# Kernel optimization log

Hardware: AMD Instinct MI355X
Metric: run time of the kernel (lower is better)

The kernel has to match this reference:

```python
import jax, jax.numpy as jnp
import numpy as np

N = 50000      # users
F_IN = 768     # input features
H = 128        # hidden_dimension == linear_channels
E = 400000     # edges per relation
SQRT_D = float(np.sqrt(H))  # heads=1 -> d = H


def leaky_relu(x):
    return jnp.where(x >= 0, x, 0.01 * x)


def hgt_layer(x, edge_list, Wk, bk, Wq, bq, Wv, bv, rel_params, Wa, ba, skip):
    # x: [N, H]; edge_list: list of [2, E] int arrays (row0=src, row1=dst)
    n = x.shape[0]
    k = x @ Wk + bk
    q = x @ Wq + bq
    v = x @ Wv + bv
    out = jnp.zeros_like(x)
    for ei, (A, M, p) in zip(edge_list, rel_params):
        src, dst = ei[0], ei[1]
        kr = (k @ A)[src]                                  # [E, H] gather
        vr = (v @ M)[src]                                  # [E, H] gather
        alpha = jnp.sum(q[dst] * kr, axis=-1) * p[0] / SQRT_D  # [E]
        amax = jax.ops.segment_max(alpha, dst, num_segments=n)
        ex = jnp.exp(alpha - amax[dst])
        denom = jax.ops.segment_sum(ex, dst, num_segments=n)
        w = ex / denom[dst]                                # segment softmax per dst
        out = out + jax.ops.segment_sum(vr * w[:, None], dst, num_segments=n)
    out = jax.nn.gelu(out, approximate=False) @ Wa + ba
    beta = jax.nn.sigmoid(skip[0])                          # learnable skip gate
    return beta * out + (1.0 - beta) * x


def setup_inputs() -> dict:
    key = jax.random.key(0)
    ks = jax.random.split(key, 16)
    d = {}
    d['features'] = jax.random.normal(ks[0], (N, F_IN), dtype=jnp.float32)
    d['edge_index0'] = jax.random.randint(ks[1], (2, E), 0, N, dtype=jnp.int64)
    d['edge_index1'] = jax.random.randint(ks[2], (2, E), 0, N, dtype=jnp.int64)
    d['W1'] = jax.random.normal(ks[3], (F_IN, H), dtype=jnp.float32) / np.sqrt(F_IN)
    d['b1'] = jnp.zeros((H,), jnp.float32)
    d['Wk'] = jax.random.normal(ks[4], (H, H), dtype=jnp.float32) / np.sqrt(H)
    d['bk'] = jnp.zeros((H,), jnp.float32)
    d['Wq'] = jax.random.normal(ks[5], (H, H), dtype=jnp.float32) / np.sqrt(H)
    d['bq'] = jnp.zeros((H,), jnp.float32)
    d['Wv'] = jax.random.normal(ks[6], (H, H), dtype=jnp.float32) / np.sqrt(H)
    d['bv'] = jnp.zeros((H,), jnp.float32)
    d['A0'] = jax.random.normal(ks[7], (H, H), dtype=jnp.float32) / np.sqrt(H)
    d['M0'] = jax.random.normal(ks[8], (H, H), dtype=jnp.float32) / np.sqrt(H)
    d['p0'] = jnp.ones((1,), jnp.float32)
    d['A1'] = jax.random.normal(ks[9], (H, H), dtype=jnp.float32) / np.sqrt(H)
    d['M1'] = jax.random.normal(ks[10], (H, H), dtype=jnp.float32) / np.sqrt(H)
    d['p1'] = jnp.ones((1,), jnp.float32)
    d['Wa'] = jax.random.normal(ks[11], (H, H), dtype=jnp.float32) / np.sqrt(H)
    d['ba'] = jnp.zeros((H,), jnp.float32)
    d['skip'] = jnp.ones((1,), jnp.float32)
    d['Wo1'] = jax.random.normal(ks[12], (H, 64), dtype=jnp.float32) / np.sqrt(H)
    d['bo1'] = jnp.zeros((64,), jnp.float32)
    d['Wo2'] = jax.random.normal(ks[13], (64, 2), dtype=jnp.float32) / np.sqrt(64)
    d['bo2'] = jnp.zeros((2,), jnp.float32)
    return d


def reference(features, edge_index0, edge_index1, W1, b1, Wk, bk, Wq, bq, Wv, bv,
              A0, M0, p0, A1, M1, p1, Wa, ba, skip, Wo1, bo1, Wo2, bo2):
    edges = [edge_index0, edge_index1]
    rel_params = [(A0, M0, p0), (A1, M1, p1)]
    # linear1 + LeakyReLU (dropout is identity in eval mode)
    x = leaky_relu(features @ W1 + b1)
    # HGT_layer1 applied twice (as in the original forward)
    x = hgt_layer(x, edges, Wk, bk, Wq, bq, Wv, bv, rel_params, Wa, ba, skip)
    x = hgt_layer(x, edges, Wk, bk, Wq, bq, Wv, bv, rel_params, Wa, ba, skip)
    x = leaky_relu(x @ Wo1 + bo1)
    return x @ Wo2 + bo2
```

## Files before the change

### kernel.cpp

```cpp
#include <hip/hip_runtime.h>
#include <math.h>

#define NNODES 50000
#define FIN 768
#define HDIM 128
#define NEDGE 400000
#define NSB 49

typedef _Float16 half8 __attribute__((ext_vector_type(8)));
typedef _Float16 half4 __attribute__((ext_vector_type(4)));
typedef _Float16 half2v __attribute__((ext_vector_type(2)));
typedef float f32x4 __attribute__((ext_vector_type(4)));

__device__ __forceinline__ void gld_lds16(const void* g, void* l) {
    __builtin_amdgcn_global_load_lds((const __attribute__((address_space(1))) unsigned int*)g,
                                     (__attribute__((address_space(3))) unsigned int*)l, 16, 0, 0);
}


__global__ __launch_bounds__(256) void count2_kernel(const int* __restrict__ ei0, const int* __restrict__ ei1,
                                                     int* __restrict__ deg0, int* __restrict__ deg1) {
    int e = blockIdx.x * 256 + threadIdx.x;
    const int* ei = blockIdx.y ? ei1 : ei0;
    int* deg = blockIdx.y ? deg1 : deg0;
    if (e < NEDGE) atomicAdd(&deg[ei[NEDGE + e]], 1);
}

__global__ __launch_bounds__(1024) void scan1_kernel(const int* __restrict__ deg0, const int* __restrict__ deg1,
                                                     int* __restrict__ ptr0, int* __restrict__ ptr1,
                                                     int* __restrict__ sums) {
    const int r = blockIdx.y;
    const int* deg = r ? deg1 : deg0;
    int* ptr = r ? ptr1 : ptr0;
    const int b = blockIdx.x, t = threadIdx.x, i = b * 1024 + t;
    __shared__ int buf[1024];
    int v = (i < NNODES) ? deg[i] : 0;
    buf[t] = v;
    __syncthreads();
    for (int off = 1; off < 1024; off <<= 1) {
        int x = (t >= off) ? buf[t - off] : 0;
        __syncthreads();
        buf[t] += x;
        __syncthreads();
    }
    if (i < NNODES) ptr[i] = buf[t] - v;
    if (t == 1023) sums[r * 64 + b] = buf[1023];
}

__global__ __launch_bounds__(64) void scan2_kernel(int* __restrict__ sums,
                                                   int* __restrict__ ptr0, int* __restrict__ ptr1) {
    const int r = blockIdx.x, t = threadIdx.x;
    int orig = (t < NSB) ? sums[r * 64 + t] : 0;
    int v = orig;
    #pragma unroll
    for (int off = 1; off < 64; off <<= 1) {
        int u = __shfl_up(v, off, 64);
        if (t >= off) v += u;
    }
    if (t < NSB) sums[r * 64 + t] = v - orig;
    if (t == NSB - 1) (r ? ptr1 : ptr0)[NNODES] = v;
}

__global__ __launch_bounds__(1024) void scan3_kernel(const int* __restrict__ sums,
                                                     int* __restrict__ ptr0, int* __restrict__ ptr1) {
    const int r = blockIdx.y;
    int* ptr = r ? ptr1 : ptr0;
    const int i = blockIdx.x * 1024 + threadIdx.x;
    if (i < NNODES) ptr[i] += sums[r * 64 + blockIdx.x];
}

__global__ __launch_bounds__(256) void scatter2_kernel(const int* __restrict__ ei0, const int* __restrict__ ei1,
                                                       const int* __restrict__ ptr0, const int* __restrict__ ptr1,
                                                       int* __restrict__ fill0, int* __restrict__ fill1,
                                                       int* __restrict__ csr0, int* __restrict__ csr1) {
    int e = blockIdx.x * 256 + threadIdx.x;
    const int* ei = blockIdx.y ? ei1 : ei0;
    const int* ptr = blockIdx.y ? ptr1 : ptr0;
    int* fill = blockIdx.y ? fill1 : fill0;
    int* csr = blockIdx.y ? csr1 : csr0;
    if (e < NEDGE) {
        int s = ei[e], d = ei[NEDGE + e];
        int p = atomicAdd(&fill[d], 1);
        csr[ptr[d] + p] = s;
    }
}

__global__ __launch_bounds__(256) void gemm_cmb_kernel(
    const float* __restrict__ Wk, const float* __restrict__ Wv,
    const float* __restrict__ A0v, const float* __restrict__ M0v,
    const float* __restrict__ A1v, const float* __restrict__ M1v,
    float* __restrict__ WkA0, float* __restrict__ WvM0,
    float* __restrict__ WkA1, float* __restrict__ WvM1)
{
    const int z = blockIdx.z;
    const float* A = (z & 1) ? Wv : Wk;
    const float* B = (z == 0) ? A0v : (z == 1) ? M0v : (z == 2) ? A1v : M1v;
    float* C = (z == 0) ? WkA0 : (z == 1) ? WvM0 : (z == 2) ? WkA1 : WvM1;
    const int M = 128, N = 128, K = 128;
    __shared__ float As[16][64];
    __shared__ float Bs[16][64];
    const int t = threadIdx.x;
    const int tx = t & 15, ty = t >> 4;
    const int bm = blockIdx.x * 64, bn = blockIdx.y * 64;
    const int ar = t >> 2, ac = (t & 3) << 2;
    const int br = t >> 4, bc = (t & 15) << 2;
    float acc[4][4] = {};
    for (int kb = 0; kb < K; kb += 16) {
        float4 av = *reinterpret_cast<const float4*>(A + (size_t)(bm + ar) * K + kb + ac);
        float4 bv = *reinterpret_cast<const float4*>(B + (size_t)(kb + br) * N + bn + bc);
        __syncthreads();
        As[ac + 0][ar] = av.x; As[ac + 1][ar] = av.y; As[ac + 2][ar] = av.z; As[ac + 3][ar] = av.w;
        *reinterpret_cast<float4*>(&Bs[br][bc]) = bv;
        __syncthreads();
        #pragma unroll
        for (int kk = 0; kk < 16; ++kk) {
            float4 a = *reinterpret_cast<const float4*>(&As[kk][ty << 2]);
            float4 b = *reinterpret_cast<const float4*>(&Bs[kk][tx << 2]);
            float am[4] = {a.x, a.y, a.z, a.w};
            float bb[4] = {b.x, b.y, b.z, b.w};
            #pragma unroll
            for (int i = 0; i < 4; ++i)
                #pragma unroll
                for (int j = 0; j < 4; ++j)
                    acc[i][j] = fmaf(am[i], bb[j], acc[i][j]);
        }
    }
    #pragma unroll
    for (int i = 0; i < 4; ++i)
        #pragma unroll
        for (int j = 0; j < 4; ++j)
            C[(size_t)(bm + (ty << 2) + i) * N + bn + (tx << 2) + j] = acc[i][j];
}

__global__ __launch_bounds__(128) void bias_cmb_kernel(
    const float* __restrict__ bk, const float* __restrict__ bv,
    const float* __restrict__ A0v, const float* __restrict__ M0v,
    const float* __restrict__ A1v, const float* __restrict__ M1v,
    float* __restrict__ bqkv)
{
    const int z = blockIdx.x;
    const int j = threadIdx.x;
    const float* b = (z & 1) ? bv : bk;
    const float* Mtx = (z == 0) ? A0v : (z == 1) ? M0v : (z == 2) ? A1v : M1v;
    float s = 0.f;
    for (int i = 0; i < HDIM; ++i) s += b[i] * Mtx[i * HDIM + j];
    const int r = z >> 1, kv = z & 1;
    bqkv[128 + r * 256 + ((j >> 1) << 2) + (kv << 1) + (j & 1)] = s;
}

__global__ __launch_bounds__(128) void pack_qkvT(
    const float* __restrict__ Wq,   const float* __restrict__ WkA0, const float* __restrict__ WvM0,
    const float* __restrict__ WkA1, const float* __restrict__ WvM1,
    const float* __restrict__ bq,
    _Float16* __restrict__ WT, float* __restrict__ bb)
{
    int n = blockIdx.x;
    int k = threadIdx.x;
    int seg = n >> 7, col = n & 127;
    const float* W = (seg == 0) ? Wq : (seg == 1) ? WkA0 : (seg == 2) ? WvM0 : (seg == 3) ? WkA1 : WvM1;
    int np;
    if (seg == 0) np = col;
    else {
        int r = (seg - 1) >> 1, kv = (seg - 1) & 1;
        np = 128 + r * 256 + ((col >> 1) << 2) + (kv << 1) + (col & 1);
    }
    WT[(size_t)np * 128 + k] = (_Float16)W[(size_t)k * 128 + col];
    if (seg == 0 && k == 0) bb[col] = bq[col];
}

__global__ void transpose_h(const float* __restrict__ W, _Float16* __restrict__ WT, int K, int N) {
    int n = blockIdx.x, k = threadIdx.x;
    WT[(size_t)n * K + k] = (_Float16)W[(size_t)k * N + n];
}

template<int MODE, bool A_F32, bool GELU>
__global__ __launch_bounds__(256) void gemm_h(
    const void* __restrict__ Av, const _Float16* __restrict__ Bt,
    const float* __restrict__ bias, const _Float16* __restrict__ Dh,
    const float* __restrict__ gate, _Float16* __restrict__ C,
    int M, int N, int K)
{
    __shared__ _Float16 sA[4096];
    __shared__ _Float16 sB[4096];
    const int t = threadIdx.x;
    const int w = t >> 6, lane = t & 63;
    const int wm = w >> 1, wn = w & 1;
    const int bm = blockIdx.x * 128, bn = blockIdx.y * 128;
    const f32x4 zero = {0.f, 0.f, 0.f, 0.f};
    f32x4 acc[4][4];
    #pragma unroll
    for (int i = 0; i < 4; ++i)
        #pragma unroll
        for (int j = 0; j < 4; ++j) acc[i][j] = zero;

    for (int kb = 0; kb < K; kb += 32) {
        #pragma unroll
        for (int it = 0; it < 2; ++it) {
            const int c = it * 256 + t;
            const int l = c & 63;
            const int row = ((c >> 6) << 4) | (l & 15);
            const int kc = (l >> 4) << 3;
            const int cb = it * 256 + (t & 192);
            int arow = bm + row; if (arow > M - 1) arow = M - 1;
            int brow = bn + row; if (brow > N - 1) brow = N - 1;
            if (A_F32) {
                const float* ap = (const float*)Av + (size_t)arow * K + kb + kc;
                f32x4 v0 = *(const f32x4*)ap;
                f32x4 v1 = *(const f32x4*)(ap + 4);
                float tmp[8] = {v0[0], v0[1], v0[2], v0[3], v1[0], v1[1], v1[2], v1[3]};
                half8 av;
                #pragma unroll
                for (int j = 0; j < 8; ++j) {
                    float x = tmp[j];
                    if (GELU) x = 0.5f * x * (1.0f + erff(x * 0.70710678118654752f));
                    av[j] = (_Float16)x;
                }
                *(half8*)(sA + (size_t)c * 8) = av;
            } else {
                gld_lds16((const _Float16*)Av + (size_t)arow * K + kb + kc, sA + (size_t)cb * 8);
            }
            gld_lds16(Bt + (size_t)brow * K + kb + kc, sB + (size_t)cb * 8);
        }
        __syncthreads();
        half8 af[4], bf[4];
        #pragma unroll
        for (int i = 0; i < 4; ++i) af[i] = *(const half8*)(sA + ((size_t)((wm * 4 + i) * 64 + lane)) * 8);
        #pragma unroll
        for (int i = 0; i < 4; ++i) bf[i] = *(const half8*)(sB + ((size_t)((wn * 4 + i) * 64 + lane)) * 8);
        #pragma unroll
        for (int i = 0; i < 4; ++i)
            #pragma unroll
            for (int j = 0; j < 4; ++j)
                acc[i][j] = __builtin_amdgcn_mfma_f32_16x16x32_f16(af[i], bf[j], acc[i][j], 0, 0, 0);
        __syncthreads();
    }

    float be = 0.f;
    if (MODE == 2) be = 1.0f / (1.0f + __expf(-gate[0]));
    const int crow0 = bm + wm * 64;
    const int ccol0 = bn + wn * 64;
    #pragma unroll
    for (int i = 0; i < 4; ++i) {
        #pragma unroll
        for (int j = 0; j < 4; ++j) {
            const int col = ccol0 + j * 16 + (lane & 15);
            if (col >= N) continue;
            #pragma unroll
            for (int r = 0; r < 4; ++r) {
                const int row = crow0 + i * 16 + ((lane >> 4) << 2) + r;
                if (row >= M) continue;
                float val = acc[i][j][r] + bias[col];
                if (MODE == 1) val = (val >= 0.f) ? val : 0.01f * val;
                if (MODE == 2) val = be * val + (1.f - be) * (float)Dh[(size_t)row * HDIM + col];
                C[(size_t)row * N + col] = (_Float16)val;
            }
        }
    }
}

__global__ __launch_bounds__(256) void attn2_kernel(
    const _Float16* __restrict__ qkv,
    const int* __restrict__ ptr0, const int* __restrict__ csr0,
    const int* __restrict__ ptr1, const int* __restrict__ csr1,
    const float* __restrict__ p0, const float* __restrict__ p1,
    float* __restrict__ att)
{
    const int w = (blockIdx.x * 256 + threadIdx.x) >> 6;
    if (w >= NNODES) return;
    const int lane = threadIdx.x & 63;
    half2v qh = *(const half2v*)(qkv + (size_t)w * 640 + (lane << 1));
    const float qx = (float)qh[0], qy = (float)qh[1];
    float ox = 0.f, oy = 0.f;
    #pragma unroll
    for (int r = 0; r < 2; ++r) {
        const int* ptrv = r ? ptr1 : ptr0;
        const int* csr  = r ? csr1 : csr0;
        const float scale = (r ? p1[0] : p0[0]) * 0.08838834764831845f;
        const int start = ptrv[w], end = ptrv[w + 1];
        if (start == end) continue;
        const _Float16* tbl = qkv + 128 + 256 * r + (lane << 2);
        float denom = 0.f, ax = 0.f, ay = 0.f;
        int i = start;
        for (; i + 4 <= end; i += 4) {
            const int s0 = csr[i], s1 = csr[i + 1], s2 = csr[i + 2], s3 = csr[i + 3];
            half4 kv0 = *(const half4*)(tbl + (size_t)s0 * 640);
            half4 kv1 = *(const half4*)(tbl + (size_t)s1 * 640);
            half4 kv2 = *(const half4*)(tbl + (size_t)s2 * 640);
            half4 kv3 = *(const half4*)(tbl + (size_t)s3 * 640);
            float d0 = qx * (float)kv0[0] + qy * (float)kv0[1];
            float d1 = qx * (float)kv1[0] + qy * (float)kv1[1];
            float d2 = qx * (float)kv2[0] + qy * (float)kv2[1];
            float d3 = qx * (float)kv3[0] + qy * (float)kv3[1];
            #pragma unroll
            for (int o2 = 32; o2; o2 >>= 1) {
                d0 += __shfl_xor(d0, o2, 64);
                d1 += __shfl_xor(d1, o2, 64);
                d2 += __shfl_xor(d2, o2, 64);
                d3 += __shfl_xor(d3, o2, 64);
            }
            const float e0 = __expf(d0 * scale), e1 = __expf(d1 * scale);
            const float e2 = __expf(d2 * scale), e3 = __expf(d3 * scale);
            denom += (e0 + e1) + (e2 + e3);
            ax += e0 * (float)kv0[2] + e1 * (float)kv1[2] + e2 * (float)kv2[2] + e3 * (float)kv3[2];
            ay += e0 * (float)kv0[3] + e1 * (float)kv1[3] + e2 * (float)kv2[3] + e3 * (float)kv3[3];
        }
        for (; i < end; ++i) {
            const int s = csr[i];
            half4 kv = *(const half4*)(tbl + (size_t)s * 640);
            float d = qx * (float)kv[0] + qy * (float)kv[1];
            #pragma unroll
            for (int o2 = 32; o2; o2 >>= 1) d += __shfl_xor(d, o2, 64);
            const float e = __expf(d * scale);
            denom += e;
            ax += e * (float)kv[2];
            ay += e * (float)kv[3];
        }
        const float inv = 1.0f / denom;
        ox += ax * inv; oy += ay * inv;
    }
    *reinterpret_cast<float2*>(att + (size_t)w * HDIM + (lane << 1)) = make_float2(ox, oy);
}

__global__ __launch_bounds__(256) void head2_kernel(const _Float16* __restrict__ h,
                                                    const float* __restrict__ Wo2,
                                                    const float* __restrict__ bo2,
                                                    float* __restrict__ out)
{
    int i = blockIdx.x * 256 + threadIdx.x;
    if (i >= NNODES) return;
    const _Float16* hp = h + (size_t)i * 64;
    float s0 = bo2[0], s1 = bo2[1];
    #pragma unroll
    for (int j0 = 0; j0 < 64; j0 += 8) {
        half8 hv = *(const half8*)(hp + j0);
        #pragma unroll
        for (int j = 0; j < 8; ++j) {
            float v = (float)hv[j];
            s0 += v * Wo2[2 * (j0 + j)];
            s1 += v * Wo2[2 * (j0 + j) + 1];
        }
    }
    out[2 * i] = s0;
    out[2 * i + 1] = s1;
}


extern "C" void kernel_launch(void* const* d_in, const int* in_sizes, int n_in,
                              void* d_out, int out_size, void* d_ws, size_t ws_size,
                              hipStream_t stream)
{
    const float* features = (const float*)d_in[0];
    const int* ei0 = (const int*)d_in[1];
    const int* ei1 = (const int*)d_in[2];
    const float* W1 = (const float*)d_in[3];
    const float* b1 = (const float*)d_in[4];
    const float* Wk = (const float*)d_in[5];
    const float* bk = (const float*)d_in[6];
    const float* Wq = (const float*)d_in[7];
    const float* bq = (const float*)d_in[8];
    const float* Wv = (const float*)d_in[9];
    const float* bv = (const float*)d_in[10];
    const float* A0 = (const float*)d_in[11];
    const float* M0 = (const float*)d_in[12];
    const float* p0 = (const float*)d_in[13];
    const float* A1 = (const float*)d_in[14];
    const float* M1 = (const float*)d_in[15];
    const float* p1 = (const float*)d_in[16];
    const float* Wa = (const float*)d_in[17];
    const float* ba = (const float*)d_in[18];
    const float* skip = (const float*)d_in[19];
    const float* Wo1 = (const float*)d_in[20];
    const float* bo1 = (const float*)d_in[21];
    const float* Wo2 = (const float*)d_in[22];
    const float* bo2 = (const float*)d_in[23];
    (void)in_sizes; (void)n_in; (void)out_size; (void)ws_size;

    char* base = (char*)d_ws;
    size_t off = 0;
    auto alloc = [&](size_t bytes) { size_t r = off; off = (off + bytes + 255) & ~(size_t)255; return base + r; };

    _Float16* x0h  = (_Float16*)alloc((size_t)NNODES * HDIM * 2);
    _Float16* x1h  = (_Float16*)alloc((size_t)NNODES * HDIM * 2);
    _Float16* qkv  = (_Float16*)alloc((size_t)NNODES * 640 * 2);
    float*    att  = (float*)   alloc((size_t)NNODES * HDIM * 4);
    _Float16* hh   = (_Float16*)alloc((size_t)NNODES * 64 * 2);
    float* WkA[2]  = { (float*)alloc(65536), (float*)alloc(65536) };
    float* WvM[2]  = { (float*)alloc(65536), (float*)alloc(65536) };
    _Float16* WqkvT = (_Float16*)alloc(640 * 128 * 2);
    float*    bqkv  = (float*)   alloc(640 * 4);
    _Float16* W1T   = (_Float16*)alloc(128 * 768 * 2);
    _Float16* WaT   = (_Float16*)alloc(128 * 128 * 2);
    _Float16* Wo1T  = (_Float16*)alloc(64 * 128 * 2);
    int* deg[2]  = { (int*)alloc(NNODES * 4), (int*)alloc(NNODES * 4) };
    int* ptrv[2] = { (int*)alloc((NNODES + 1) * 4), (int*)alloc((NNODES + 1) * 4) };
    int* fill[2] = { (int*)alloc(NNODES * 4), (int*)alloc(NNODES * 4) };
    int* csr[2]  = { (int*)alloc(NEDGE * 4),  (int*)alloc(NEDGE * 4) };
    int* sums    = (int*)alloc(2 * 64 * 4);

    hipMemsetAsync(deg[0], 0, NNODES * 4, stream);
    hipMemsetAsync(deg[1], 0, NNODES * 4, stream);
    hipMemsetAsync(fill[0], 0, NNODES * 4, stream);
    hipMemsetAsync(fill[1], 0, NNODES * 4, stream);
    const int egrid = (NEDGE + 255) / 256;
    count2_kernel<<<dim3(egrid, 2), 256, 0, stream>>>(ei0, ei1, deg[0], deg[1]);
    scan1_kernel<<<dim3(NSB, 2), 1024, 0, stream>>>(deg[0], deg[1], ptrv[0], ptrv[1], sums);
    scan2_kernel<<<2, 64, 0, stream>>>(sums, ptrv[0], ptrv[1]);
    scan3_kernel<<<dim3(NSB, 2), 1024, 0, stream>>>(sums, ptrv[0], ptrv[1]);
    scatter2_kernel<<<dim3(egrid, 2), 256, 0, stream>>>(ei0, ei1, ptrv[0], ptrv[1],
                                                        fill[0], fill[1], csr[0], csr[1]);

    gemm_cmb_kernel<<<dim3(2, 2, 4), 256, 0, stream>>>(Wk, Wv, A0, M0, A1, M1,
                                                       WkA[0], WvM[0], WkA[1], WvM[1]);
    bias_cmb_kernel<<<4, 128, 0, stream>>>(bk, bv, A0, M0, A1, M1, bqkv);

    pack_qkvT<<<640, 128, 0, stream>>>(Wq, WkA[0], WvM[0], WkA[1], WvM[1], bq, WqkvT, bqkv);
    transpose_h<<<128, 768, 0, stream>>>(W1, W1T, 768, 128);
    transpose_h<<<128, 128, 0, stream>>>(Wa, WaT, 128, 128);
    transpose_h<<<64, 128, 0, stream>>>(Wo1, Wo1T, 128, 64);

    const int MBLK = (NNODES + 127) / 128;

    gemm_h<1, true, false><<<dim3(MBLK, 1), 256, 0, stream>>>(
        features, W1T, b1, nullptr, nullptr, x0h, NNODES, HDIM, FIN);

    _Float16* xin = x0h;
    _Float16* xout = x1h;
    for (int layer = 0; layer < 2; ++layer) {
        gemm_h<0, false, false><<<dim3(MBLK, 5), 256, 0, stream>>>(
            xin, WqkvT, bqkv, nullptr, nullptr, qkv, NNODES, 640, HDIM);
        attn2_kernel<<<(NNODES * 64 + 255) / 256, 256, 0, stream>>>(
            qkv, ptrv[0], csr[0], ptrv[1], csr[1], p0, p1, att);
        gemm_h<2, true, true><<<dim3(MBLK, 1), 256, 0, stream>>>(
            att, WaT, ba, xin, skip, xout, NNODES, HDIM, HDIM);
        _Float16* tmp = xin; xin = xout; xout = tmp;
    }

    gemm_h<1, false, false><<<dim3(MBLK, 1), 256, 0, stream>>>(
        xin, Wo1T, bo1, nullptr, nullptr, hh, NNODES, 64, HDIM);
    head2_kernel<<<(NNODES + 255) / 256, 256, 0, stream>>>(hh, Wo2, bo2, (float*)d_out);
}
```

Before: 496.4 us.

## Add 32-row-tile GEMM kernel for narrow-N GEMMs to increase block count

Adds a gemm_h32 kernel that computes 32-row by 128-column tiles with four waves, each owning 32 output columns. It replaces the 128-row-tile GEMM for the input projection, the post-attention GELU/Wa/skip GEMM and the Wo1 head GEMM. The goal is to raise the number of blocks from about 391 to about 1563 so the GPU's compute units are better filled on these skinny GEMMs. In exchange, the weight tile is fetched again by every block, there is no double buffering, and the N=64 GEMM leaves half the waves doing discarded work.

```diff
diff --git a/kernel.cpp b/kernel.cpp
--- a/kernel.cpp
+++ b/kernel.cpp
@@ -258,6 +258,94 @@
     }
 }
 
+template<int MODE, bool A_F32, bool GELU>
+__global__ __launch_bounds__(256) void gemm_h32(
+    const void* __restrict__ Av, const _Float16* __restrict__ Bt,
+    const float* __restrict__ bias, const _Float16* __restrict__ Dh,
+    const float* __restrict__ gate, _Float16* __restrict__ C,
+    int M, int N, int K)
+{
+    __shared__ _Float16 sA[4 * 64 * 8];
+    __shared__ _Float16 sB[16 * 64 * 8];
+    const int t = threadIdx.x;
+    const int w = t >> 6, lane = t & 63;
+    const int rl = lane & 15, kg = lane >> 4;
+    const int bm = blockIdx.x * 32;
+    const f32x4 zero = {0.f, 0.f, 0.f, 0.f};
+    f32x4 acc[2][2] = {{zero, zero}, {zero, zero}};
+
+    for (int kb = 0; kb < K; kb += 64) {
+        {
+            const int mi = w >> 1, kk = w & 1;
+            int arow = bm + mi * 16 + rl; if (arow > M - 1) arow = M - 1;
+            const int ko = kb + kk * 32 + kg * 8;
+            if (A_F32) {
+                const float* ap = (const float*)Av + (size_t)arow * K + ko;
+                f32x4 v0 = *(const f32x4*)ap;
+                f32x4 v1 = *(const f32x4*)(ap + 4);
+                float tmp[8] = {v0[0], v0[1], v0[2], v0[3], v1[0], v1[1], v1[2], v1[3]};
+                half8 av;
+                #pragma unroll
+                for (int j = 0; j < 8; ++j) {
+                    float x = tmp[j];
+                    if (GELU) x = 0.5f * x * (1.0f + erff(x * 0.70710678118654752f));
+                    av[j] = (_Float16)x;
+                }
+                *(half8*)(sA + (size_t)(w * 64 + lane) * 8) = av;
+            } else {
+                gld_lds16((const _Float16*)Av + (size_t)arow * K + ko, sA + (size_t)(w * 64) * 8);
+            }
+        }
+        #pragma unroll
+        for (int j = 0; j < 4; ++j) {
+            const int fb = w * 4 + j;
+            const int ni = (j >> 1) & 1, kk = j & 1;
+            int nrow = w * 32 + ni * 16 + rl; if (nrow > N - 1) nrow = N - 1;
+            gld_lds16(Bt + (size_t)nrow * K + kb + kk * 32 + kg * 8, sB + (size_t)(fb * 64) * 8);
+        }
+        __syncthreads();
+        half8 af[2][2], bf[2][2];
+        #pragma unroll
+        for (int mi = 0; mi < 2; ++mi)
+            #pragma unroll
+            for (int kk = 0; kk < 2; ++kk)
+                af[mi][kk] = *(const half8*)(sA + (size_t)((mi * 2 + kk) * 64 + lane) * 8);
+        #pragma unroll
+        for (int ni = 0; ni < 2; ++ni)
+            #pragma unroll
+            for (int kk = 0; kk < 2; ++kk)
+                bf[ni][kk] = *(const half8*)(sB + (size_t)((w * 4 + ni * 2 + kk) * 64 + lane) * 8);
+        #pragma unroll
+        for (int mi = 0; mi < 2; ++mi)
+            #pragma unroll
+            for (int ni = 0; ni < 2; ++ni)
+                #pragma unroll
+                for (int kk = 0; kk < 2; ++kk)
+                    acc[mi][ni] = __builtin_amdgcn_mfma_f32_16x16x32_f16(af[mi][kk], bf[ni][kk], acc[mi][ni], 0, 0, 0);
+        __syncthreads();
+    }
+
+    float be = 0.f;
+    if (MODE == 2) be = 1.0f / (1.0f + __expf(-gate[0]));
+    #pragma unroll
+    for (int mi = 0; mi < 2; ++mi) {
+        #pragma unroll
+        for (int ni = 0; ni < 2; ++ni) {
+            const int col = w * 32 + ni * 16 + rl;
+            if (col >= N) continue;
+            #pragma unroll
+            for (int r = 0; r < 4; ++r) {
+                const int row = bm + mi * 16 + kg * 4 + r;
+                if (row >= M) continue;
+                float val = acc[mi][ni][r] + bias[col];
+                if (MODE == 1) val = (val >= 0.f) ? val : 0.01f * val;
+                if (MODE == 2) val = be * val + (1.f - be) * (float)Dh[(size_t)row * HDIM + col];
+                C[(size_t)row * N + col] = (_Float16)val;
+            }
+        }
+    }
+}
+
 __global__ __launch_bounds__(256) void attn2_kernel(
     const _Float16* __restrict__ qkv,
     const int* __restrict__ ptr0, const int* __restrict__ csr0,
@@ -419,8 +507,9 @@
     transpose_h<<<64, 128, 0, stream>>>(Wo1, Wo1T, 128, 64);
 
     const int MBLK = (NNODES + 127) / 128;
-
-    gemm_h<1, true, false><<<dim3(MBLK, 1), 256, 0, stream>>>(
+    const int MBLK32 = (NNODES + 31) / 32;
+
+    gemm_h32<1, true, false><<<MBLK32, 256, 0, stream>>>(
         features, W1T, b1, nullptr, nullptr, x0h, NNODES, HDIM, FIN);
 
     _Float16* xin = x0h;
@@ -430,12 +519,12 @@
             xin, WqkvT, bqkv, nullptr, nullptr, qkv, NNODES, 640, HDIM);
         attn2_kernel<<<(NNODES * 64 + 255) / 256, 256, 0, stream>>>(
             qkv, ptrv[0], csr[0], ptrv[1], csr[1], p0, p1, att);
-        gemm_h<2, true, true><<<dim3(MBLK, 1), 256, 0, stream>>>(
+        gemm_h32<2, true, true><<<MBLK32, 256, 0, stream>>>(
             att, WaT, ba, xin, skip, xout, NNODES, HDIM, HDIM);
         _Float16* tmp = xin; xin = xout; xout = tmp;
     }
 
-    gemm_h<1, false, false><<<dim3(MBLK, 1), 256, 0, stream>>>(
+    gemm_h32<1, false, false><<<MBLK32, 256, 0, stream>>>(
         xin, Wo1T, bo1, nullptr, nullptr, hh, NNODES, 64, HDIM);
     head2_kernel<<<(NNODES + 255) / 256, 256, 0, stream>>>(hh, Wo2, bo2, (float*)d_out);
 }
```

After: 482.3 us. -2.8%, faster.

## Replace LDS-staged GEMM with direct-from-global MFMA GEMM using 32-row tiles

Applied to the files above, without the earlier changes.

The shared-memory tiled 128x128 GEMM is replaced by a kernel where each wave loads its A and B fragments straight from global memory into registers and issues MFMAs, with no LDS staging and no barriers. Tiles shrink to 32 rows per block with each wave owning 32 columns, and K becomes a compile-time template parameter. This removes LDS traffic and syncs and raises the block count for these skinny GEMMs. In exchange it gives up reuse of B across waves through LDS, relying on L1/L2 caching, and the GELU on A is now recomputed for every column-block of waves that reads the same rows.

```diff
diff --git a/kernel.cpp b/kernel.cpp
--- a/kernel.cpp
+++ b/kernel.cpp
@@ -12,9 +12,16 @@
 typedef _Float16 half2v __attribute__((ext_vector_type(2)));
 typedef float f32x4 __attribute__((ext_vector_type(4)));
 
-__device__ __forceinline__ void gld_lds16(const void* g, void* l) {
-    __builtin_amdgcn_global_load_lds((const __attribute__((address_space(1))) unsigned int*)g,
-                                     (__attribute__((address_space(3))) unsigned int*)l, 16, 0, 0);
+template<bool GELU>
+__device__ __forceinline__ half8 cvt8(f32x4 v0, f32x4 v1) {
+    half8 av;
+    #pragma unroll
+    for (int j = 0; j < 8; ++j) {
+        float x = (j < 4) ? v0[j] : v1[j - 4];
+        if (GELU) x = 0.5f * x * (1.0f + erff(x * 0.70710678118654752f));
+        av[j] = (_Float16)x;
+    }
+    return av;
 }
 
 
@@ -96,7 +103,7 @@
     const float* A = (z & 1) ? Wv : Wk;
     const float* B = (z == 0) ? A0v : (z == 1) ? M0v : (z == 2) ? A1v : M1v;
     float* C = (z == 0) ? WkA0 : (z == 1) ? WvM0 : (z == 2) ? WkA1 : WvM1;
-    const int M = 128, N = 128, K = 128;
+    const int N = 128, K = 128;
     __shared__ float As[16][64];
     __shared__ float Bs[16][64];
     const int t = threadIdx.x;
@@ -173,83 +180,65 @@
     WT[(size_t)n * K + k] = (_Float16)W[(size_t)k * N + n];
 }
 
-template<int MODE, bool A_F32, bool GELU>
-__global__ __launch_bounds__(256) void gemm_h(
+template<int MODE, bool A_F32, bool GELU, int KLEN>
+__global__ __launch_bounds__(256) void gemm_direct(
     const void* __restrict__ Av, const _Float16* __restrict__ Bt,
     const float* __restrict__ bias, const _Float16* __restrict__ Dh,
     const float* __restrict__ gate, _Float16* __restrict__ C,
-    int M, int N, int K)
-{
-    __shared__ _Float16 sA[4096];
-    __shared__ _Float16 sB[4096];
+    int M, int N)
+{
     const int t = threadIdx.x;
     const int w = t >> 6, lane = t & 63;
-    const int wm = w >> 1, wn = w & 1;
-    const int bm = blockIdx.x * 128, bn = blockIdx.y * 128;
+    const int rl = lane & 15, kg = lane >> 4;
+    const int bm = blockIdx.x * 32;
+    const int bn = blockIdx.y * 128 + w * 32;
+
+    int arow[2], bcol[2];
+    #pragma unroll
+    for (int mi = 0; mi < 2; ++mi) { int rr = bm + mi * 16 + rl; arow[mi] = (rr < M) ? rr : M - 1; }
+    #pragma unroll
+    for (int ni = 0; ni < 2; ++ni) { int cc = bn + ni * 16 + rl; bcol[ni] = (cc < N) ? cc : N - 1; }
+
     const f32x4 zero = {0.f, 0.f, 0.f, 0.f};
-    f32x4 acc[4][4];
-    #pragma unroll
-    for (int i = 0; i < 4; ++i)
-        #pragma unroll
-        for (int j = 0; j < 4; ++j) acc[i][j] = zero;
-
-    for (int kb = 0; kb < K; kb += 32) {
-        #pragma unroll
-        for (int it = 0; it < 2; ++it) {
-            const int c = it * 256 + t;
-            const int l = c & 63;
-            const int row = ((c >> 6) << 4) | (l & 15);
-            const int kc = (l >> 4) << 3;
-            const int cb = it * 256 + (t & 192);
-            int arow = bm + row; if (arow > M - 1) arow = M - 1;
-            int brow = bn + row; if (brow > N - 1) brow = N - 1;
+    f32x4 acc[2][2] = {{zero, zero}, {zero, zero}};
+    const int koff = kg << 3;
+
+    #pragma unroll 4
+    for (int kt = 0; kt < KLEN / 32; ++kt) {
+        const int k = (kt << 5) + koff;
+        half8 a[2], b[2];
+        #pragma unroll
+        for (int mi = 0; mi < 2; ++mi) {
             if (A_F32) {
-                const float* ap = (const float*)Av + (size_t)arow * K + kb + kc;
-                f32x4 v0 = *(const f32x4*)ap;
-                f32x4 v1 = *(const f32x4*)(ap + 4);
-                float tmp[8] = {v0[0], v0[1], v0[2], v0[3], v1[0], v1[1], v1[2], v1[3]};
-                half8 av;
-                #pragma unroll
-                for (int j = 0; j < 8; ++j) {
-                    float x = tmp[j];
-                    if (GELU) x = 0.5f * x * (1.0f + erff(x * 0.70710678118654752f));
-                    av[j] = (_Float16)x;
-                }
-                *(half8*)(sA + (size_t)c * 8) = av;
+                const float* ap = (const float*)Av + (size_t)arow[mi] * KLEN + k;
+                a[mi] = cvt8<GELU>(*(const f32x4*)ap, *(const f32x4*)(ap + 4));
             } else {
-                gld_lds16((const _Float16*)Av + (size_t)arow * K + kb + kc, sA + (size_t)cb * 8);
+                a[mi] = *(const half8*)((const _Float16*)Av + (size_t)arow[mi] * KLEN + k);
             }
-            gld_lds16(Bt + (size_t)brow * K + kb + kc, sB + (size_t)cb * 8);
-        }
-        __syncthreads();
-        half8 af[4], bf[4];
-        #pragma unroll
-        for (int i = 0; i < 4; ++i) af[i] = *(const half8*)(sA + ((size_t)((wm * 4 + i) * 64 + lane)) * 8);
-        #pragma unroll
-        for (int i = 0; i < 4; ++i) bf[i] = *(const half8*)(sB + ((size_t)((wn * 4 + i) * 64 + lane)) * 8);
-        #pragma unroll
-        for (int i = 0; i < 4; ++i)
+        }
+        #pragma unroll
+        for (int ni = 0; ni < 2; ++ni)
+            b[ni] = *(const half8*)(Bt + (size_t)bcol[ni] * KLEN + k);
+        #pragma unroll
+        for (int mi = 0; mi < 2; ++mi)
             #pragma unroll
-            for (int j = 0; j < 4; ++j)
-                acc[i][j] = __builtin_amdgcn_mfma_f32_16x16x32_f16(af[i], bf[j], acc[i][j], 0, 0, 0);
-        __syncthreads();
+            for (int ni = 0; ni < 2; ++ni)
+                acc[mi][ni] = __builtin_amdgcn_mfma_f32_16x16x32_f16(a[mi], b[ni], acc[mi][ni], 0, 0, 0);
     }
 
     float be = 0.f;
     if (MODE == 2) be = 1.0f / (1.0f + __expf(-gate[0]));
-    const int crow0 = bm + wm * 64;
-    const int ccol0 = bn + wn * 64;
-    #pragma unroll
-    for (int i = 0; i < 4; ++i) {
-        #pragma unroll
-        for (int j = 0; j < 4; ++j) {
-            const int col = ccol0 + j * 16 + (lane & 15);
+    #pragma unroll
+    for (int mi = 0; mi < 2; ++mi) {
+        #pragma unroll
+        for (int ni = 0; ni < 2; ++ni) {
+            const int col = bn + ni * 16 + rl;
             if (col >= N) continue;
             #pragma unroll
             for (int r = 0; r < 4; ++r) {
-                const int row = crow0 + i * 16 + ((lane >> 4) << 2) + r;
+                const int row = bm + mi * 16 + (kg << 2) + r;
                 if (row >= M) continue;
-                float val = acc[i][j][r] + bias[col];
+                float val = acc[mi][ni][r] + bias[col];
                 if (MODE == 1) val = (val >= 0.f) ? val : 0.01f * val;
                 if (MODE == 2) val = be * val + (1.f - be) * (float)Dh[(size_t)row * HDIM + col];
                 C[(size_t)row * N + col] = (_Float16)val;
@@ -418,24 +407,24 @@
     transpose_h<<<128, 128, 0, stream>>>(Wa, WaT, 128, 128);
     transpose_h<<<64, 128, 0, stream>>>(Wo1, Wo1T, 128, 64);
 
-    const int MBLK = (NNODES + 127) / 128;
-
-    gemm_h<1, true, false><<<dim3(MBLK, 1), 256, 0, stream>>>(
-        features, W1T, b1, nullptr, nullptr, x0h, NNODES, HDIM, FIN);
+    const int MBLK32 = (NNODES + 31) / 32;
+
+    gemm_direct<1, true, false, FIN><<<dim3(MBLK32, 1), 256, 0, stream>>>(
+        features, W1T, b1, nullptr, nullptr, x0h, NNODES, HDIM);
 
     _Float16* xin = x0h;
     _Float16* xout = x1h;
     for (int layer = 0; layer < 2; ++layer) {
-        gemm_h<0, false, false><<<dim3(MBLK, 5), 256, 0, stream>>>(
-            xin, WqkvT, bqkv, nullptr, nullptr, qkv, NNODES, 640, HDIM);
+        gemm_direct<0, false, false, HDIM><<<dim3(MBLK32, 5), 256, 0, stream>>>(
+            xin, WqkvT, bqkv, nullptr, nullptr, qkv, NNODES, 640);
         attn2_kernel<<<(NNODES * 64 + 255) / 256, 256, 0, stream>>>(
             qkv, ptrv[0], csr[0], ptrv[1], csr[1], p0, p1, att);
-        gemm_h<2, true, true><<<dim3(MBLK, 1), 256, 0, stream>>>(
-            att, WaT, ba, xin, skip, xout, NNODES, HDIM, HDIM);
+        gemm_direct<2, true, true, HDIM><<<dim3(MBLK32, 1), 256, 0, stream>>>(
+            att, WaT, ba, xin, skip, xout, NNODES, HDIM);
         _Float16* tmp = xin; xin = xout; xout = tmp;
     }
 
-    gemm_h<1, false, false><<<dim3(MBLK, 1), 256, 0, stream>>>(
-        xin, Wo1T, bo1, nullptr, nullptr, hh, NNODES, 64, HDIM);
+    gemm_direct<1, false, false, HDIM><<<dim3(MBLK32, 1), 256, 0, stream>>>(
+        xin, Wo1T, bo1, nullptr, nullptr, hh, NNODES, 64);
     head2_kernel<<<(NNODES + 255) / 256, 256, 0, stream>>>(hh, Wo2, bo2, (float*)d_out);
 }
```

Measured after the change: 599.2 us. +20.7%, slower.
